# Optimization experiments

Measured on AMD Instinct MI355X. Metric: run time of the kernel, lower is better.

The kernel has to match this reference:

```python
import jax, jax.numpy as jnp
import numpy as np

B, C, CI, H, W = 4, 128, 64, 64, 64


def conv1x1(x, w, b):
    # x: [B,C,H,W], w: [Cout,Cin], b: [Cout]
    return jnp.einsum('bchw,oc->bohw', x, w) + b[None, :, None, None]


def setup_inputs() -> dict:
    key = jax.random.key(0)
    ks = jax.random.split(key, 10)
    s = 0.05  # keep logits in a sane range for softmax
    return {
        'x0': jax.random.normal(ks[0], (B, C, H, W), jnp.float32),
        'x1': jax.random.normal(ks[1], (B, C, H, W), jnp.float32),
        'g_w': jax.random.normal(ks[2], (CI, C), jnp.float32) * s,
        'g_b': jax.random.normal(ks[3], (CI,), jnp.float32) * s,
        'theta_w': jax.random.normal(ks[4], (CI, C), jnp.float32) * s,
        'theta_b': jax.random.normal(ks[5], (CI,), jnp.float32) * s,
        'phi_w': jax.random.normal(ks[6], (CI, C), jnp.float32) * s,
        'phi_b': jax.random.normal(ks[7], (CI,), jnp.float32) * s,
        'W_w': jax.random.normal(ks[8], (C, CI), jnp.float32) * s,
        'W_b': jax.random.normal(ks[9], (C,), jnp.float32) * s,
    }


def reference(x0, x1, g_w, g_b, theta_w, theta_b, phi_w, phi_b, W_w, W_b):
    b, c, h, w = x0.shape
    n = h * w
    ci = g_w.shape[0]
    g_x = conv1x1(x0, g_w, g_b).reshape(b, ci, n).transpose(0, 2, 1)      # [B,N,Ci]
    theta_x = conv1x1(x1, theta_w, theta_b).reshape(b, ci, n).transpose(0, 2, 1)  # [B,N,Ci]
    phi_x = conv1x1(x0, phi_w, phi_b).reshape(b, ci, n)                    # [B,Ci,N]
    f = jnp.einsum('bqc,bck->bqk', theta_x, phi_x)                         # [B,N,N]
    f_div_C = jax.nn.softmax(f, axis=-1)
    y = jnp.einsum('bqk,bkc->bqc', f_div_C, g_x)                           # [B,N,Ci]
    y = y.transpose(0, 2, 1).reshape(b, ci, h, w)
    W_y = conv1x1(y, W_w, W_b)
    return W_y + x0
```

## Files before the change

kernel.cpp:

```cpp
#include <hip/hip_runtime.h>
#include <hip/hip_bf16.h>


typedef unsigned int   u32;
typedef unsigned short u16;
typedef __attribute__((ext_vector_type(8))) short short8;
typedef __attribute__((ext_vector_type(4))) short short4v;
typedef __attribute__((ext_vector_type(4))) float f32x4;

#define LOG2E 1.4426950408889634f
#define KSPLIT 8

__device__ __forceinline__ float b2f(u16 v) {
  union { u32 u; float f; } x; x.u = ((u32)v) << 16; return x.f;
}
__device__ __forceinline__ u16 f2b(float f) {
  u32 u = __float_as_uint(f);
  return (u16)((u + 0x8000u) >> 16);
}
__device__ __forceinline__ short8 load_w_frag(const float* p, float s) {
  const float4 f0 = ((const float4*)p)[0];
  const float4 f1 = ((const float4*)p)[1];
  union { u32 w[4]; short8 s8; } r;
  r.w[0] = (u32)f2b(f0.x * s) | ((u32)f2b(f0.y * s) << 16);
  r.w[1] = (u32)f2b(f0.z * s) | ((u32)f2b(f0.w * s) << 16);
  r.w[2] = (u32)f2b(f1.x * s) | ((u32)f2b(f1.y * s) << 16);
  r.w[3] = (u32)f2b(f1.z * s) | ((u32)f2b(f1.w * s) << 16);
  return r.s8;
}


__global__ __launch_bounds__(256) void qkv_fused_kernel(
    const float* __restrict__ x0, const float* __restrict__ x1,
    const float* __restrict__ tw, const float* __restrict__ tb,
    const float* __restrict__ pw, const float* __restrict__ pb,
    const float* __restrict__ gw, const float* __restrict__ gb,
    u16* __restrict__ Q, u16* __restrict__ K, u16* __restrict__ Vt)
{
  const int n0 = blockIdx.x * 64;
  const int b  = blockIdx.y;
  const int t  = threadIdx.x;

  __shared__ __align__(16) short xt[2][64][136];

  #pragma unroll
  for (int i = 0; i < 16; ++i) {
    const int idx = i * 256 + t;
    const int tensor = idx >> 11;
    const int c  = (idx >> 4) & 127;
    const int n4 = idx & 15;
    const float4 v = *(const float4*)(
        (tensor ? x1 : x0) + ((size_t)b * 128 + c) * 4096 + n0 + n4 * 4);
    short* d = &xt[tensor][n4 * 4][c];
    d[0]       = (short)f2b(v.x);
    d[136]     = (short)f2b(v.y);
    d[2 * 136] = (short)f2b(v.z);
    d[3 * 136] = (short)f2b(v.w);
  }
  asm volatile("" ::: "memory");
  __syncthreads();

  const int wave = t >> 6;
  const int lane = t & 63;
  const int quad = lane >> 4, l15 = lane & 15;

  if (wave < 2) {
    const int conv = wave;
    const float* wsrc = conv ? pw : tw;
    const float  ws   = conv ? 1.f : LOG2E;
    const short* xl   = &xt[conv ? 0 : 1][0][0];

    f32x4 acc[4][4];
    #pragma unroll
    for (int i = 0; i < 4; ++i)
      #pragma unroll
      for (int j = 0; j < 4; ++j) acc[i][j] = (f32x4){0.f, 0.f, 0.f, 0.f};

    #pragma unroll
    for (int kk = 0; kk < 4; ++kk) {
      short8 wf[4], xf[4];
      #pragma unroll
      for (int ot = 0; ot < 4; ++ot)
        wf[ot] = load_w_frag(wsrc + (ot * 16 + l15) * 128 + kk * 32 + quad * 8, ws);
      #pragma unroll
      for (int nt = 0; nt < 4; ++nt)
        xf[nt] = *(const short8*)(xl + (nt * 16 + l15) * 136 + kk * 32 + quad * 8);
      #pragma unroll
      for (int i = 0; i < 4; ++i)
        #pragma unroll
        for (int j = 0; j < 4; ++j)
          acc[i][j] = __builtin_amdgcn_mfma_f32_16x16x32_bf16(xf[i], wf[j], acc[i][j], 0, 0, 0);
    }

    u16* dst = (conv ? K : Q) + (size_t)b * 4096 * 64;
    const float* bias = conv ? pb : tb;
    const float bscale = conv ? 1.f : LOG2E;
    #pragma unroll
    for (int ot = 0; ot < 4; ++ot) {
      const float bv = bias[ot * 16 + l15] * bscale;
      #pragma unroll
      for (int nt = 0; nt < 4; ++nt)
        #pragma unroll
        for (int r = 0; r < 4; ++r) {
          const int n = n0 + nt * 16 + quad * 4 + r;
          dst[(size_t)n * 64 + ot * 16 + l15] = f2b(acc[nt][ot][r] + bv);
        }
    }
  } else {
    const int oh = wave - 2;
    const short* xl = &xt[0][0][0];

    f32x4 acc[2][4];
    #pragma unroll
    for (int i = 0; i < 2; ++i)
      #pragma unroll
      for (int j = 0; j < 4; ++j) acc[i][j] = (f32x4){0.f, 0.f, 0.f, 0.f};

    #pragma unroll
    for (int kk = 0; kk < 4; ++kk) {
      short8 wf[2], xf[4];
      #pragma unroll
      for (int ot = 0; ot < 2; ++ot)
        wf[ot] = load_w_frag(gw + ((oh * 2 + ot) * 16 + l15) * 128 + kk * 32 + quad * 8, 1.f);
      #pragma unroll
      for (int nt = 0; nt < 4; ++nt)
        xf[nt] = *(const short8*)(xl + (nt * 16 + l15) * 136 + kk * 32 + quad * 8);
      #pragma unroll
      for (int i = 0; i < 2; ++i)
        #pragma unroll
        for (int j = 0; j < 4; ++j)
          acc[i][j] = __builtin_amdgcn_mfma_f32_16x16x32_bf16(wf[i], xf[j], acc[i][j], 0, 0, 0);
    }

    u16* dst = Vt + (size_t)b * 64 * 4096;
    #pragma unroll
    for (int ot = 0; ot < 2; ++ot)
      #pragma unroll
      for (int r = 0; r < 4; ++r) {
        const int o = (oh * 2 + ot) * 16 + quad * 4 + r;
        const float bv = gb[o];
        #pragma unroll
        for (int nc = 0; nc < 4; ++nc)
          dst[(size_t)o * 4096 + n0 + nc * 16 + l15] = f2b(acc[ot][nc][r] + bv);
      }
  }
}

__global__ __launch_bounds__(256, 4) void attn_kernel(
    const u16* __restrict__ Q, const u16* __restrict__ K,
    const u16* __restrict__ Vt, u16* __restrict__ Opart,
    float* __restrict__ Lp)
{
  const int qt = blockIdx.x, b = blockIdx.y, ks = blockIdx.z;
  const int tid  = threadIdx.x;
  const int wave = tid >> 6;
  const int lane = tid & 63;
  const int quad = lane >> 4;
  const int l15  = lane & 15;

  __shared__ __align__(16) short K_lds[64][72];
  __shared__ __align__(16) short V_lds[64][72];
  __shared__ __align__(16) short P_lds[4][32][40];
  short* pw = &P_lds[wave][0][0];

  const int q0 = qt * 128 + wave * 32;
  const u16* Qb = Q  + (size_t)b * 4096 * 64;
  const u16* Kb = K  + (size_t)b * 4096 * 64;
  const u16* Vb = Vt + (size_t)b * 64 * 4096;

  const int kbase = ks * (4096 / KSPLIT);
  const int NKT   = 4096 / KSPLIT / 64;

  const int sr = tid >> 2;
  const int sc = (tid & 3) * 8;

  short8 qf[2][2];
  #pragma unroll
  for (int nt = 0; nt < 2; ++nt) {
    const u16* qp = Qb + (size_t)(q0 + nt * 16 + l15) * 64 + quad * 8;
    qf[nt][0] = *(const short8*)qp;
    qf[nt][1] = *(const short8*)(qp + 32);
  }

  f32x4 oacc[2][4];
  #pragma unroll
  for (int i = 0; i < 2; ++i)
    #pragma unroll
    for (int j = 0; j < 4; ++j)
      oacc[i][j] = (f32x4){0.f, 0.f, 0.f, 0.f};
  float lsum[2] = {0.f, 0.f};

  {
    const u16* kg = Kb + (size_t)kbase * 64;
    uint4 ka = *(const uint4*)(kg + (size_t)sr * 64 + sc);
    uint4 kb = *(const uint4*)(kg + (size_t)sr * 64 + sc + 32);
    uint4 va = *(const uint4*)(Vb + (size_t)sr * 4096 + kbase + sc);
    uint4 vb = *(const uint4*)(Vb + (size_t)sr * 4096 + kbase + sc + 32);
    *(uint4*)&K_lds[sr][sc]      = ka;
    *(uint4*)&K_lds[sr][sc + 32] = kb;
    *(uint4*)&V_lds[sr][sc]      = va;
    *(uint4*)&V_lds[sr][sc + 32] = vb;
  }
  __syncthreads();

  for (int kt = 0; kt < NKT; ++kt) {
    const bool pre = (kt + 1 < NKT);

    uint4 ka, kb, va, vb;
    if (pre) {
      const int k1 = kbase + (kt + 1) * 64;
      const u16* kg = Kb + (size_t)k1 * 64;
      ka = *(const uint4*)(kg + (size_t)sr * 64 + sc);
      kb = *(const uint4*)(kg + (size_t)sr * 64 + sc + 32);
      va = *(const uint4*)(Vb + (size_t)sr * 4096 + k1 + sc);
      vb = *(const uint4*)(Vb + (size_t)sr * 4096 + k1 + sc + 32);
    }

    #pragma unroll
    for (int kh = 0; kh < 2; ++kh) {
      short8 kf[2][2], vf[4];
      #pragma unroll
      for (int m = 0; m < 2; ++m) {
        kf[m][0] = *(const short8*)&K_lds[(kh * 2 + m) * 16 + l15][quad * 8];
        kf[m][1] = *(const short8*)&K_lds[(kh * 2 + m) * 16 + l15][quad * 8 + 32];
      }
      #pragma unroll
      for (int nd = 0; nd < 4; ++nd)
        vf[nd] = *(const short8*)&V_lds[nd * 16 + l15][kh * 32 + quad * 8];

      #pragma unroll
      for (int m = 0; m < 2; ++m) {
        #pragma unroll
        for (int nt = 0; nt < 2; ++nt) {
          f32x4 s = {0.f, 0.f, 0.f, 0.f};
          s = __builtin_amdgcn_mfma_f32_16x16x32_bf16(kf[m][0], qf[nt][0], s, 0, 0, 0);
          s = __builtin_amdgcn_mfma_f32_16x16x32_bf16(kf[m][1], qf[nt][1], s, 0, 0, 0);
          float p0 = exp2f(s[0]), p1 = exp2f(s[1]), p2 = exp2f(s[2]), p3 = exp2f(s[3]);
          lsum[nt] += (p0 + p1) + (p2 + p3);
          u32 u0 = __float_as_uint(p0) + 0x8000u;
          u32 u1 = __float_as_uint(p1) + 0x8000u;
          u32 u2 = __float_as_uint(p2) + 0x8000u;
          u32 u3 = __float_as_uint(p3) + 0x8000u;
          union { uint2 u; short4v s4; } pk;
          pk.u.x = __builtin_amdgcn_perm(u1, u0, 0x07060302u);
          pk.u.y = __builtin_amdgcn_perm(u3, u2, 0x07060302u);
          *(short4v*)(pw + (nt * 16 + l15) * 40 + m * 16 + quad * 4) = pk.s4;
        }
      }

      asm volatile("" ::: "memory");

      #pragma unroll
      for (int mq = 0; mq < 2; ++mq) {
        const short8 pa = *(const short8*)(pw + (mq * 16 + l15) * 40 + quad * 8);
        #pragma unroll
        for (int nd = 0; nd < 4; ++nd)
          oacc[mq][nd] = __builtin_amdgcn_mfma_f32_16x16x32_bf16(pa, vf[nd], oacc[mq][nd], 0, 0, 0);
      }

      asm volatile("" ::: "memory");
    }

    __syncthreads();
    if (pre) {
      *(uint4*)&K_lds[sr][sc]      = ka;
      *(uint4*)&K_lds[sr][sc + 32] = kb;
      *(uint4*)&V_lds[sr][sc]      = va;
      *(uint4*)&V_lds[sr][sc + 32] = vb;
      __syncthreads();
    }
  }

  #pragma unroll
  for (int nt = 0; nt < 2; ++nt) {
    float v = lsum[nt];
    v += __shfl_xor(v, 16, 64);
    v += __shfl_xor(v, 32, 64);
    lsum[nt] = v;
  }
  float* LpB = Lp + ((size_t)ks * 4 + b) * 4096;
  if (quad == 0) {
    #pragma unroll
    for (int nt = 0; nt < 2; ++nt)
      LpB[q0 + nt * 16 + l15] = lsum[nt];
  }

  u16* Ob = Opart + ((size_t)ks * 4 + b) * 4096 * 64;
  #pragma unroll
  for (int mq = 0; mq < 2; ++mq)
    #pragma unroll
    for (int nd = 0; nd < 4; ++nd)
      #pragma unroll
      for (int r = 0; r < 4; ++r) {
        int q = q0 + mq * 16 + quad * 4 + r;
        Ob[(size_t)q * 64 + nd * 16 + l15] = f2b(oacc[mq][nd][r]);
      }
}

__global__ __launch_bounds__(256) void out_fused_kernel(
    const u16* __restrict__ Opart, const float* __restrict__ Lp,
    const float* __restrict__ Wf, const float* __restrict__ Wbf,
    const float* __restrict__ x0, float* __restrict__ out)
{
  const int n0 = blockIdx.x * 64;
  const int b  = blockIdx.y;
  const int t  = threadIdx.x;

  __shared__ __align__(16) short Ys[64][72];

  {
    const int nl = t >> 2;
    const int q4 = t & 3;
    const int ng = n0 + nl;

    float l = 0.f;
    #pragma unroll
    for (int ks = 0; ks < KSPLIT; ++ks)
      l += Lp[((size_t)ks * 4 + b) * 4096 + ng];

    float a[16];
    #pragma unroll
    for (int j = 0; j < 16; ++j) a[j] = 0.f;
    #pragma unroll
    for (int ks = 0; ks < KSPLIT; ++ks) {
      const uint4* row = (const uint4*)(Opart + (((size_t)ks * 4 + b) * 4096 + ng) * 64 + q4 * 16);
      #pragma unroll
      for (int v = 0; v < 2; ++v) {
        uint4 r = row[v];
        u32 wds[4] = {r.x, r.y, r.z, r.w};
        #pragma unroll
        for (int j = 0; j < 4; ++j) {
          a[v * 8 + 2 * j]     += __uint_as_float(wds[j] << 16);
          a[v * 8 + 2 * j + 1] += __uint_as_float(wds[j] & 0xffff0000u);
        }
      }
    }
    const float rinv = 1.f / l;
    union { u32 w[8]; short8 s8[2]; } pk;
    #pragma unroll
    for (int j = 0; j < 8; ++j)
      pk.w[j] = (u32)f2b(a[2 * j] * rinv) | ((u32)f2b(a[2 * j + 1] * rinv) << 16);
    *(short8*)&Ys[nl][q4 * 16]     = pk.s8[0];
    *(short8*)&Ys[nl][q4 * 16 + 8] = pk.s8[1];
  }
  asm volatile("" ::: "memory");
  __syncthreads();

  const int wave = t >> 6;
  const int lane = t & 63;
  const int quad = lane >> 4, l15 = lane & 15;

  f32x4 acc[2][4];
  #pragma unroll
  for (int i = 0; i < 2; ++i)
    #pragma unroll
    for (int j = 0; j < 4; ++j) acc[i][j] = (f32x4){0.f, 0.f, 0.f, 0.f};

  #pragma unroll
  for (int kk = 0; kk < 2; ++kk) {
    short8 wf[2], yf[4];
    #pragma unroll
    for (int ot = 0; ot < 2; ++ot)
      wf[ot] = load_w_frag(Wf + ((wave * 2 + ot) * 16 + l15) * 64 + kk * 32 + quad * 8, 1.f);
    #pragma unroll
    for (int nt = 0; nt < 4; ++nt)
      yf[nt] = *(const short8*)&Ys[nt * 16 + l15][kk * 32 + quad * 8];
    #pragma unroll
    for (int i = 0; i < 2; ++i)
      #pragma unroll
      for (int j = 0; j < 4; ++j)
        acc[i][j] = __builtin_amdgcn_mfma_f32_16x16x32_bf16(wf[i], yf[j], acc[i][j], 0, 0, 0);
  }

  #pragma unroll
  for (int ot = 0; ot < 2; ++ot)
    #pragma unroll
    for (int r = 0; r < 4; ++r) {
      const int o = (wave * 2 + ot) * 16 + quad * 4 + r;
      const float bv = Wbf[o];
      #pragma unroll
      for (int nt = 0; nt < 4; ++nt) {
        const size_t idx = ((size_t)(b * 128 + o)) * 4096 + n0 + nt * 16 + l15;
        out[idx] = acc[ot][nt][r] + bv + x0[idx];
      }
    }
}

extern "C" void kernel_launch(void* const* d_in, const int* in_sizes, int n_in,
                              void* d_out, int out_size, void* d_ws, size_t ws_size,
                              hipStream_t stream) {
  const float* x0 = (const float*)d_in[0];
  const float* x1 = (const float*)d_in[1];
  const float* gw = (const float*)d_in[2];
  const float* gb = (const float*)d_in[3];
  const float* tw = (const float*)d_in[4];
  const float* tb = (const float*)d_in[5];
  const float* pw = (const float*)d_in[6];
  const float* pb = (const float*)d_in[7];
  const float* Ww = (const float*)d_in[8];
  const float* Wb = (const float*)d_in[9];
  float* out = (float*)d_out;

  char* ws = (char*)d_ws;
  u16*   Qw    = (u16*)(ws + 0);
  u16*   Kw    = (u16*)(ws + (2u << 20));
  u16*   Vtw   = (u16*)(ws + (4u << 20));
  u16*   Opart = (u16*)(ws + (6u << 20));
  float* Lp    = (float*)(ws + (22u << 20));

  qkv_fused_kernel<<<dim3(64, 4), dim3(256), 0, stream>>>(
      x0, x1, tw, tb, pw, pb, gw, gb, Qw, Kw, Vtw);

  attn_kernel<<<dim3(32, 4, KSPLIT), dim3(256), 0, stream>>>(Qw, Kw, Vtw, Opart, Lp);

  out_fused_kernel<<<dim3(64, 4), dim3(256), 0, stream>>>(
      Opart, Lp, Ww, Wb, x0, out);
}
```

Baseline: 128.4 us.

## Halve pixel tile in QKV and output kernels, add MFMA priority in attention

The QKV projection and output kernels now process 32 pixels per block instead of 64, which doubles the grid to 512 blocks so more of the GPU's compute units are occupied. The QKV staging load is rewritten to read four channels per thread and store packed 4-wide bf16 vectors to shared memory instead of scalar shorts. The attention kernel raises wave priority with s_setprio around the P·V MFMA block. In exchange, the projection and output weight fragments are reloaded by twice as many blocks.

```diff
diff --git a/kernel.cpp b/kernel.cpp
--- a/kernel.cpp
+++ b/kernel.cpp
@@ -37,25 +37,34 @@
     const float* __restrict__ gw, const float* __restrict__ gb,
     u16* __restrict__ Q, u16* __restrict__ K, u16* __restrict__ Vt)
 {
-  const int n0 = blockIdx.x * 64;
+  const int n0 = blockIdx.x * 32;
   const int b  = blockIdx.y;
   const int t  = threadIdx.x;
 
-  __shared__ __align__(16) short xt[2][64][136];
-
-  #pragma unroll
-  for (int i = 0; i < 16; ++i) {
-    const int idx = i * 256 + t;
-    const int tensor = idx >> 11;
-    const int c  = (idx >> 4) & 127;
-    const int n4 = idx & 15;
-    const float4 v = *(const float4*)(
-        (tensor ? x1 : x0) + ((size_t)b * 128 + c) * 4096 + n0 + n4 * 4);
-    short* d = &xt[tensor][n4 * 4][c];
-    d[0]       = (short)f2b(v.x);
-    d[136]     = (short)f2b(v.y);
-    d[2 * 136] = (short)f2b(v.z);
-    d[3 * 136] = (short)f2b(v.w);
+  __shared__ __align__(16) short xt[2][32][136];
+
+  {
+    const int cg = (t >> 3) & 31;
+    const int ng = t & 7;
+    #pragma unroll
+    for (int k = 0; k < 2; ++k) {
+      const float* src = (k ? x1 : x0) + ((size_t)b * 128 + cg * 4) * 4096 + n0 + ng * 4;
+      float4 v0 = *(const float4*)(src);
+      float4 v1 = *(const float4*)(src + 4096);
+      float4 v2 = *(const float4*)(src + 2 * 4096);
+      float4 v3 = *(const float4*)(src + 3 * 4096);
+      const float c0[4] = {v0.x, v0.y, v0.z, v0.w};
+      const float c1[4] = {v1.x, v1.y, v1.z, v1.w};
+      const float c2[4] = {v2.x, v2.y, v2.z, v2.w};
+      const float c3[4] = {v3.x, v3.y, v3.z, v3.w};
+      #pragma unroll
+      for (int j = 0; j < 4; ++j) {
+        union { u32 w[2]; short4v s4; } pk;
+        pk.w[0] = (u32)f2b(c0[j]) | ((u32)f2b(c1[j]) << 16);
+        pk.w[1] = (u32)f2b(c2[j]) | ((u32)f2b(c3[j]) << 16);
+        *(short4v*)&xt[k][ng * 4 + j][cg * 4] = pk.s4;
+      }
+    }
   }
   asm volatile("" ::: "memory");
   __syncthreads();
@@ -70,23 +79,23 @@
     const float  ws   = conv ? 1.f : LOG2E;
     const short* xl   = &xt[conv ? 0 : 1][0][0];
 
-    f32x4 acc[4][4];
-    #pragma unroll
-    for (int i = 0; i < 4; ++i)
+    f32x4 acc[2][4];
+    #pragma unroll
+    for (int i = 0; i < 2; ++i)
       #pragma unroll
       for (int j = 0; j < 4; ++j) acc[i][j] = (f32x4){0.f, 0.f, 0.f, 0.f};
 
     #pragma unroll
     for (int kk = 0; kk < 4; ++kk) {
-      short8 wf[4], xf[4];
+      short8 wf[4], xf[2];
       #pragma unroll
       for (int ot = 0; ot < 4; ++ot)
         wf[ot] = load_w_frag(wsrc + (ot * 16 + l15) * 128 + kk * 32 + quad * 8, ws);
       #pragma unroll
-      for (int nt = 0; nt < 4; ++nt)
+      for (int nt = 0; nt < 2; ++nt)
         xf[nt] = *(const short8*)(xl + (nt * 16 + l15) * 136 + kk * 32 + quad * 8);
       #pragma unroll
-      for (int i = 0; i < 4; ++i)
+      for (int i = 0; i < 2; ++i)
         #pragma unroll
         for (int j = 0; j < 4; ++j)
           acc[i][j] = __builtin_amdgcn_mfma_f32_16x16x32_bf16(xf[i], wf[j], acc[i][j], 0, 0, 0);
@@ -99,7 +108,7 @@
     for (int ot = 0; ot < 4; ++ot) {
       const float bv = bias[ot * 16 + l15] * bscale;
       #pragma unroll
-      for (int nt = 0; nt < 4; ++nt)
+      for (int nt = 0; nt < 2; ++nt)
         #pragma unroll
         for (int r = 0; r < 4; ++r) {
           const int n = n0 + nt * 16 + quad * 4 + r;
@@ -110,25 +119,25 @@
     const int oh = wave - 2;
     const short* xl = &xt[0][0][0];
 
-    f32x4 acc[2][4];
+    f32x4 acc[2][2];
     #pragma unroll
     for (int i = 0; i < 2; ++i)
       #pragma unroll
-      for (int j = 0; j < 4; ++j) acc[i][j] = (f32x4){0.f, 0.f, 0.f, 0.f};
+      for (int j = 0; j < 2; ++j) acc[i][j] = (f32x4){0.f, 0.f, 0.f, 0.f};
 
     #pragma unroll
     for (int kk = 0; kk < 4; ++kk) {
-      short8 wf[2], xf[4];
+      short8 wf[2], xf[2];
       #pragma unroll
       for (int ot = 0; ot < 2; ++ot)
         wf[ot] = load_w_frag(gw + ((oh * 2 + ot) * 16 + l15) * 128 + kk * 32 + quad * 8, 1.f);
       #pragma unroll
-      for (int nt = 0; nt < 4; ++nt)
+      for (int nt = 0; nt < 2; ++nt)
         xf[nt] = *(const short8*)(xl + (nt * 16 + l15) * 136 + kk * 32 + quad * 8);
       #pragma unroll
       for (int i = 0; i < 2; ++i)
         #pragma unroll
-        for (int j = 0; j < 4; ++j)
+        for (int j = 0; j < 2; ++j)
           acc[i][j] = __builtin_amdgcn_mfma_f32_16x16x32_bf16(wf[i], xf[j], acc[i][j], 0, 0, 0);
     }
 
@@ -140,7 +149,7 @@
         const int o = (oh * 2 + ot) * 16 + quad * 4 + r;
         const float bv = gb[o];
         #pragma unroll
-        for (int nc = 0; nc < 4; ++nc)
+        for (int nc = 0; nc < 2; ++nc)
           dst[(size_t)o * 4096 + n0 + nc * 16 + l15] = f2b(acc[ot][nc][r] + bv);
       }
   }
@@ -250,6 +259,7 @@
 
       asm volatile("" ::: "memory");
 
+      __builtin_amdgcn_s_setprio(1);
       #pragma unroll
       for (int mq = 0; mq < 2; ++mq) {
         const short8 pa = *(const short8*)(pw + (mq * 16 + l15) * 40 + quad * 8);
@@ -257,6 +267,7 @@
         for (int nd = 0; nd < 4; ++nd)
           oacc[mq][nd] = __builtin_amdgcn_mfma_f32_16x16x32_bf16(pa, vf[nd], oacc[mq][nd], 0, 0, 0);
       }
+      __builtin_amdgcn_s_setprio(0);
 
       asm volatile("" ::: "memory");
     }
@@ -302,15 +313,15 @@
     const float* __restrict__ Wf, const float* __restrict__ Wbf,
     const float* __restrict__ x0, float* __restrict__ out)
 {
-  const int n0 = blockIdx.x * 64;
+  const int n0 = blockIdx.x * 32;
   const int b  = blockIdx.y;
   const int t  = threadIdx.x;
 
-  __shared__ __align__(16) short Ys[64][72];
+  __shared__ __align__(16) short Ys[32][72];
 
   {
-    const int nl = t >> 2;
-    const int q4 = t & 3;
+    const int nl = t >> 3;
+    const int q8 = t & 7;
     const int ng = n0 + nl;
 
     float l = 0.f;
@@ -318,30 +329,25 @@
     for (int ks = 0; ks < KSPLIT; ++ks)
       l += Lp[((size_t)ks * 4 + b) * 4096 + ng];
 
-    float a[16];
-    #pragma unroll
-    for (int j = 0; j < 16; ++j) a[j] = 0.f;
+    float a[8];
+    #pragma unroll
+    for (int j = 0; j < 8; ++j) a[j] = 0.f;
     #pragma unroll
     for (int ks = 0; ks < KSPLIT; ++ks) {
-      const uint4* row = (const uint4*)(Opart + (((size_t)ks * 4 + b) * 4096 + ng) * 64 + q4 * 16);
-      #pragma unroll
-      for (int v = 0; v < 2; ++v) {
-        uint4 r = row[v];
-        u32 wds[4] = {r.x, r.y, r.z, r.w};
-        #pragma unroll
-        for (int j = 0; j < 4; ++j) {
-          a[v * 8 + 2 * j]     += __uint_as_float(wds[j] << 16);
-          a[v * 8 + 2 * j + 1] += __uint_as_float(wds[j] & 0xffff0000u);
-        }
+      uint4 r = *(const uint4*)(Opart + (((size_t)ks * 4 + b) * 4096 + ng) * 64 + q8 * 8);
+      u32 wds[4] = {r.x, r.y, r.z, r.w};
+      #pragma unroll
+      for (int j = 0; j < 4; ++j) {
+        a[2 * j]     += __uint_as_float(wds[j] << 16);
+        a[2 * j + 1] += __uint_as_float(wds[j] & 0xffff0000u);
       }
     }
     const float rinv = 1.f / l;
-    union { u32 w[8]; short8 s8[2]; } pk;
-    #pragma unroll
-    for (int j = 0; j < 8; ++j)
+    union { u32 w[4]; short8 s8; } pk;
+    #pragma unroll
+    for (int j = 0; j < 4; ++j)
       pk.w[j] = (u32)f2b(a[2 * j] * rinv) | ((u32)f2b(a[2 * j + 1] * rinv) << 16);
-    *(short8*)&Ys[nl][q4 * 16]     = pk.s8[0];
-    *(short8*)&Ys[nl][q4 * 16 + 8] = pk.s8[1];
+    *(short8*)&Ys[nl][q8 * 8] = pk.s8;
   }
   asm volatile("" ::: "memory");
   __syncthreads();
@@ -350,25 +356,25 @@
   const int lane = t & 63;
   const int quad = lane >> 4, l15 = lane & 15;
 
-  f32x4 acc[2][4];
+  f32x4 acc[2][2];
   #pragma unroll
   for (int i = 0; i < 2; ++i)
     #pragma unroll
-    for (int j = 0; j < 4; ++j) acc[i][j] = (f32x4){0.f, 0.f, 0.f, 0.f};
+    for (int j = 0; j < 2; ++j) acc[i][j] = (f32x4){0.f, 0.f, 0.f, 0.f};
 
   #pragma unroll
   for (int kk = 0; kk < 2; ++kk) {
-    short8 wf[2], yf[4];
+    short8 wf[2], yf[2];
     #pragma unroll
     for (int ot = 0; ot < 2; ++ot)
       wf[ot] = load_w_frag(Wf + ((wave * 2 + ot) * 16 + l15) * 64 + kk * 32 + quad * 8, 1.f);
     #pragma unroll
-    for (int nt = 0; nt < 4; ++nt)
+    for (int nt = 0; nt < 2; ++nt)
       yf[nt] = *(const short8*)&Ys[nt * 16 + l15][kk * 32 + quad * 8];
     #pragma unroll
     for (int i = 0; i < 2; ++i)
       #pragma unroll
-      for (int j = 0; j < 4; ++j)
+      for (int j = 0; j < 2; ++j)
         acc[i][j] = __builtin_amdgcn_mfma_f32_16x16x32_bf16(wf[i], yf[j], acc[i][j], 0, 0, 0);
   }
 
@@ -379,7 +385,7 @@
       const int o = (wave * 2 + ot) * 16 + quad * 4 + r;
       const float bv = Wbf[o];
       #pragma unroll
-      for (int nt = 0; nt < 4; ++nt) {
+      for (int nt = 0; nt < 2; ++nt) {
         const size_t idx = ((size_t)(b * 128 + o)) * 4096 + n0 + nt * 16 + l15;
         out[idx] = acc[ot][nt][r] + bv + x0[idx];
       }
@@ -408,11 +414,11 @@
   u16*   Opart = (u16*)(ws + (6u << 20));
   float* Lp    = (float*)(ws + (22u << 20));
 
-  qkv_fused_kernel<<<dim3(64, 4), dim3(256), 0, stream>>>(
+  qkv_fused_kernel<<<dim3(128, 4), dim3(256), 0, stream>>>(
       x0, x1, tw, tb, pw, pb, gw, gb, Qw, Kw, Vtw);
 
   attn_kernel<<<dim3(32, 4, KSPLIT), dim3(256), 0, stream>>>(Qw, Kw, Vtw, Opart, Lp);
 
-  out_fused_kernel<<<dim3(64, 4), dim3(256), 0, stream>>>(
+  out_fused_kernel<<<dim3(128, 4), dim3(256), 0, stream>>>(
       Opart, Lp, Ww, Wb, x0, out);
 }
```

Result: slower. 134.4 us (+4.6%).

## Double-buffer K/V in LDS and keep P in registers for PV MFMA

Applied to the files above, without the earlier changes.

Converts the K/V shared-memory tiles to double buffers so the next tile is written into the alternate buffer, cutting one __syncthreads per iteration. Removes the per-wave P staging through LDS: the exponentiated scores are packed straight into registers and used as the A operand of the PV MFMA. The V fragment reads are changed to two 4-element loads with a matching k permutation so the register-resident P layout lines up. This raises LDS use for K/V but drops the P buffer, and it relies on the MFMA k-index permutation being consistent between P and V.

```diff
diff --git a/kernel.cpp b/kernel.cpp
--- a/kernel.cpp
+++ b/kernel.cpp
@@ -158,10 +158,8 @@
   const int quad = lane >> 4;
   const int l15  = lane & 15;
 
-  __shared__ __align__(16) short K_lds[64][72];
-  __shared__ __align__(16) short V_lds[64][72];
-  __shared__ __align__(16) short P_lds[4][32][40];
-  short* pw = &P_lds[wave][0][0];
+  __shared__ __align__(16) short K_lds[2][64][72];
+  __shared__ __align__(16) short V_lds[2][64][72];
 
   const int q0 = qt * 128 + wave * 32;
   const u16* Qb = Q  + (size_t)b * 4096 * 64;
@@ -192,42 +190,49 @@
 
   {
     const u16* kg = Kb + (size_t)kbase * 64;
-    uint4 ka = *(const uint4*)(kg + (size_t)sr * 64 + sc);
-    uint4 kb = *(const uint4*)(kg + (size_t)sr * 64 + sc + 32);
-    uint4 va = *(const uint4*)(Vb + (size_t)sr * 4096 + kbase + sc);
-    uint4 vb = *(const uint4*)(Vb + (size_t)sr * 4096 + kbase + sc + 32);
-    *(uint4*)&K_lds[sr][sc]      = ka;
-    *(uint4*)&K_lds[sr][sc + 32] = kb;
-    *(uint4*)&V_lds[sr][sc]      = va;
-    *(uint4*)&V_lds[sr][sc + 32] = vb;
+    uint4 ra = *(const uint4*)(kg + (size_t)sr * 64 + sc);
+    uint4 rb = *(const uint4*)(kg + (size_t)sr * 64 + sc + 32);
+    uint4 rc = *(const uint4*)(Vb + (size_t)sr * 4096 + kbase + sc);
+    uint4 rd = *(const uint4*)(Vb + (size_t)sr * 4096 + kbase + sc + 32);
+    *(uint4*)&K_lds[0][sr][sc]      = ra;
+    *(uint4*)&K_lds[0][sr][sc + 32] = rb;
+    *(uint4*)&V_lds[0][sr][sc]      = rc;
+    *(uint4*)&V_lds[0][sr][sc + 32] = rd;
   }
   __syncthreads();
 
   for (int kt = 0; kt < NKT; ++kt) {
+    const int buf = kt & 1;
     const bool pre = (kt + 1 < NKT);
 
-    uint4 ka, kb, va, vb;
+    uint4 kra, krb, vra, vrb;
     if (pre) {
       const int k1 = kbase + (kt + 1) * 64;
       const u16* kg = Kb + (size_t)k1 * 64;
-      ka = *(const uint4*)(kg + (size_t)sr * 64 + sc);
-      kb = *(const uint4*)(kg + (size_t)sr * 64 + sc + 32);
-      va = *(const uint4*)(Vb + (size_t)sr * 4096 + k1 + sc);
-      vb = *(const uint4*)(Vb + (size_t)sr * 4096 + k1 + sc + 32);
+      kra = *(const uint4*)(kg + (size_t)sr * 64 + sc);
+      krb = *(const uint4*)(kg + (size_t)sr * 64 + sc + 32);
+      vra = *(const uint4*)(Vb + (size_t)sr * 4096 + k1 + sc);
+      vrb = *(const uint4*)(Vb + (size_t)sr * 4096 + k1 + sc + 32);
     }
 
     #pragma unroll
     for (int kh = 0; kh < 2; ++kh) {
-      short8 kf[2][2], vf[4];
+      short8 kf[2][2];
       #pragma unroll
       for (int m = 0; m < 2; ++m) {
-        kf[m][0] = *(const short8*)&K_lds[(kh * 2 + m) * 16 + l15][quad * 8];
-        kf[m][1] = *(const short8*)&K_lds[(kh * 2 + m) * 16 + l15][quad * 8 + 32];
-      }
-      #pragma unroll
-      for (int nd = 0; nd < 4; ++nd)
-        vf[nd] = *(const short8*)&V_lds[nd * 16 + l15][kh * 32 + quad * 8];
-
+        kf[m][0] = *(const short8*)&K_lds[buf][(kh * 2 + m) * 16 + l15][quad * 8];
+        kf[m][1] = *(const short8*)&K_lds[buf][(kh * 2 + m) * 16 + l15][quad * 8 + 32];
+      }
+      short8 vf[4];
+      #pragma unroll
+      for (int nd = 0; nd < 4; ++nd) {
+        union { short4v h[2]; short8 s8; } vv;
+        vv.h[0] = *(const short4v*)&V_lds[buf][nd * 16 + l15][kh * 32 + quad * 4];
+        vv.h[1] = *(const short4v*)&V_lds[buf][nd * 16 + l15][kh * 32 + 16 + quad * 4];
+        vf[nd] = vv.s8;
+      }
+
+      union { u32 w[4]; short8 s8; } pa[2];
       #pragma unroll
       for (int m = 0; m < 2; ++m) {
         #pragma unroll
@@ -241,34 +246,26 @@
           u32 u1 = __float_as_uint(p1) + 0x8000u;
           u32 u2 = __float_as_uint(p2) + 0x8000u;
           u32 u3 = __float_as_uint(p3) + 0x8000u;
-          union { uint2 u; short4v s4; } pk;
-          pk.u.x = __builtin_amdgcn_perm(u1, u0, 0x07060302u);
-          pk.u.y = __builtin_amdgcn_perm(u3, u2, 0x07060302u);
-          *(short4v*)(pw + (nt * 16 + l15) * 40 + m * 16 + quad * 4) = pk.s4;
+          pa[nt].w[m * 2]     = __builtin_amdgcn_perm(u1, u0, 0x07060302u);
+          pa[nt].w[m * 2 + 1] = __builtin_amdgcn_perm(u3, u2, 0x07060302u);
         }
       }
 
-      asm volatile("" ::: "memory");
-
-      #pragma unroll
-      for (int mq = 0; mq < 2; ++mq) {
-        const short8 pa = *(const short8*)(pw + (mq * 16 + l15) * 40 + quad * 8);
+      #pragma unroll
+      for (int nt = 0; nt < 2; ++nt)
         #pragma unroll
         for (int nd = 0; nd < 4; ++nd)
-          oacc[mq][nd] = __builtin_amdgcn_mfma_f32_16x16x32_bf16(pa, vf[nd], oacc[mq][nd], 0, 0, 0);
-      }
-
-      asm volatile("" ::: "memory");
-    }
-
+          oacc[nt][nd] = __builtin_amdgcn_mfma_f32_16x16x32_bf16(pa[nt].s8, vf[nd], oacc[nt][nd], 0, 0, 0);
+    }
+
+    if (pre) {
+      const int nb = buf ^ 1;
+      *(uint4*)&K_lds[nb][sr][sc]      = kra;
+      *(uint4*)&K_lds[nb][sr][sc + 32] = krb;
+      *(uint4*)&V_lds[nb][sr][sc]      = vra;
+      *(uint4*)&V_lds[nb][sr][sc + 32] = vrb;
+    }
     __syncthreads();
-    if (pre) {
-      *(uint4*)&K_lds[sr][sc]      = ka;
-      *(uint4*)&K_lds[sr][sc + 32] = kb;
-      *(uint4*)&V_lds[sr][sc]      = va;
-      *(uint4*)&V_lds[sr][sc + 32] = vb;
-      __syncthreads();
-    }
   }
 
   #pragma unroll
```

Result: no change. 128.7 us (+0.2%).
